# Performance work log

Measured on AMD Instinct MI355X. Metric: run time of the kernel, lower is better.

## Reference

```python
import jax, jax.numpy as jnp
import numpy as np
from jax import lax

B, CM, CQ, CO, H, W, KS = 8, 64, 64, 64, 128, 128, 3
K = KS * KS  # 9 kernel taps, offset_group=1


def setup_inputs() -> dict:
    key = jax.random.key(0)
    k1, k2, k3, k4 = jax.random.split(key, 4)
    mem = jax.random.normal(k1, (B, CM, H, W), jnp.float32)
    que = jax.random.normal(k2, (B, CQ, H, W), jnp.float32)
    # conv_offset: Conv2d(CM+CQ -> 3*K, 3x3, pad=1, bias=True); small init so offsets are a few px
    w_off = jax.random.normal(k3, (3 * K, CM + CQ, KS, KS), jnp.float32) * 0.01
    b_off = jnp.zeros((3 * K,), jnp.float32)
    # deformable conv weight: [CO, CM, 3, 3], bias=False
    w_def = jax.random.normal(k4, (CO, CM, KS, KS), jnp.float32) * (1.0 / np.sqrt(CM * K))
    return {"mem": mem, "que": que, "w_off": w_off, "b_off": b_off, "w_def": w_def}


def _deform_conv2d(mem, offset, mask, w_def):
    """Deformable conv v2 (stride=1, pad=1, dil=1, groups=1, offset_group=1).
    mem: [B,C,H,W]; offset: [B,2K,H,W] (dy,dx pairs per tap); mask: [B,K,H,W]."""
    Bn, C, Hn, Wn = mem.shape
    Kn = w_def.shape[2] * w_def.shape[3]
    off = offset.reshape(Bn, Kn, 2, Hn, Wn)
    dy, dx = off[:, :, 0], off[:, :, 1]            # [B,K,H,W]
    kk = jnp.arange(Kn)
    ky = (kk // KS - 1).astype(jnp.float32)        # kernel tap offsets with pad=1, dil=1
    kx = (kk % KS - 1).astype(jnp.float32)
    gy = jnp.arange(Hn, dtype=jnp.float32)
    gx = jnp.arange(Wn, dtype=jnp.float32)
    py = gy[None, None, :, None] + ky[None, :, None, None] + dy   # sample y coords [B,K,H,W]
    px = gx[None, None, None, :] + kx[None, :, None, None] + dx   # sample x coords [B,K,H,W]
    y0 = jnp.floor(py)
    x0 = jnp.floor(px)
    fy = py - y0
    fx = px - x0
    b_idx = jnp.arange(Bn)[:, None, None, None]

    def corner(iy, ix, wgt):
        valid = (iy >= 0) & (iy < Hn) & (ix >= 0) & (ix < Wn)  # zero padding outside
        iyc = jnp.clip(iy.astype(jnp.int32), 0, Hn - 1)
        ixc = jnp.clip(ix.astype(jnp.int32), 0, Wn - 1)
        vals = mem[b_idx, :, iyc, ixc]             # gather -> [B,K,H,W,C]
        return vals * (wgt * valid)[..., None]

    sampled = (corner(y0, x0, (1 - fy) * (1 - fx))
               + corner(y0, x0 + 1, (1 - fy) * fx)
               + corner(y0 + 1, x0, fy * (1 - fx))
               + corner(y0 + 1, x0 + 1, fy * fx))
    sampled = sampled * mask[..., None]            # modulation (applied raw, as in source)
    w = w_def.reshape(w_def.shape[0], C, Kn)       # [O,C,K]; tap order kh*KS+kw matches kk
    return jnp.einsum('bkhwc,ock->bohw', sampled, w)


def reference(mem, que, w_off, b_off, w_def):
    x = jnp.concatenate([mem, que], axis=1)
    off = lax.conv_general_dilated(
        x, w_off, window_strides=(1, 1), padding=[(1, 1), (1, 1)],
        dimension_numbers=('NCHW', 'OIHW', 'NCHW')) + b_off[None, :, None, None]
    offset, mask = off[:, :2 * K], off[:, 2 * K:]
    return _deform_conv2d(mem, offset, mask, w_def)
```

## Files before the change

### kernel.cpp

```cpp
#include <hip/hip_runtime.h>
#include <hip/hip_fp16.h>

#define Bn   8
#define CM_  64
#define CIN  128
#define CO_  64
#define Hn   128
#define Wn   128
#define Kn   9
#define COFF 27
#define HW   (Hn * Wn)

typedef __attribute__((ext_vector_type(8))) _Float16 f16x8;
typedef __attribute__((ext_vector_type(4))) float f32x4;

__device__ __forceinline__ unsigned h22u(__half2 h) {
    unsigned u; __builtin_memcpy(&u, &h, 4); return u;
}
__device__ __forceinline__ __half2 u2h2(unsigned u) {
    __half2 h; __builtin_memcpy(&h, &u, 4); return h;
}
__device__ __forceinline__ unsigned short f2h(float x) {
    __half h = __float2half(x);
    unsigned short u; __builtin_memcpy(&u, &h, 2); return u;
}

__global__ __launch_bounds__(256) void transpose_kernel(
    const float* __restrict__ mem, const float* __restrict__ que,
    uint4* __restrict__ xT4)
{
    __shared__ unsigned tile[64 * 65];

    const int bb   = blockIdx.x & 7;
    const int pix0 = (blockIdx.x >> 3) * 64;
    const int tid  = threadIdx.x;
    const int pxL  = tid & 63;
    const int cg   = tid >> 6;

    const float* mb = mem + (size_t)bb * CM_ * HW + pix0 + pxL;
    const float* qb = que + (size_t)bb * CM_ * HW + pix0 + pxL;

    #pragma unroll
    for (int i = 0; i < 16; ++i) {
        const int c = cg * 32 + 2 * i;
        const float v0 = (c < CM_) ? mb[(size_t)c * HW]       : qb[(size_t)(c - CM_) * HW];
        const float v1 = (c + 1 < CM_) ? mb[(size_t)(c + 1) * HW] : qb[(size_t)(c + 1 - CM_) * HW];
        tile[pxL * 65 + cg * 16 + i] = h22u(__floats2half2_rn(v0, v1));
    }
    __syncthreads();

    uint4* dst = xT4 + (size_t)(bb * HW + pix0) * 16;
    #pragma unroll
    for (int p = 0; p < 4; ++p) {
        const int G  = p * 256 + tid;
        const int px = G >> 4;
        const int u  = G & 15;
        uint4 v;
        v.x = tile[px * 65 + u * 4 + 0];
        v.y = tile[px * 65 + u * 4 + 1];
        v.z = tile[px * 65 + u * 4 + 2];
        v.w = tile[px * 65 + u * 4 + 3];
        dst[G] = v;
    }
}

__global__ __launch_bounds__(256) void wprep_all_kernel(
    const float* __restrict__ w_def, const float* __restrict__ w_off,
    unsigned short* __restrict__ wpd, unsigned short* __restrict__ wpo)
{
    int idx = blockIdx.x * 256 + threadIdx.x;
    if (idx < CO_ * CM_ * Kn) {
        const int j  = idx & 7;
        const int L  = (idx >> 3) & 63;
        const int f  = (idx >> 9) & 1;
        const int gk = idx >> 10;
        const int k  = gk % 9;
        const int g  = gk / 9;
        const int o  = g * 16 + (L & 15);
        const int c  = f * 32 + (L >> 4) * 8 + j;
        wpd[idx] = f2h(w_def[(size_t)(o * CM_ + c) * Kn + k]);
        return;
    }
    idx -= CO_ * CM_ * Kn;
    if (idx < 2 * 9 * 4 * 64 * 8) {
        const int j   = idx & 7;
        const int L   = (idx >> 3) & 63;
        const int s   = (idx >> 9) & 3;
        const int r   = idx >> 11;
        const int tap = r % 9;
        const int ot  = r / 9;
        const int o   = ot * 16 + (L & 15);
        const int c   = s * 32 + (L >> 4) * 8 + j;
        wpo[idx] = (o < COFF) ? f2h(w_off[(size_t)(o * CIN + c) * Kn + tap])
                              : (unsigned short)0;
    }
}

__global__ __launch_bounds__(256) void fused_deform_kernel(
    const uint4* __restrict__ xT4, const uint4* __restrict__ wpo,
    const uint4* __restrict__ wpd, const float* __restrict__ b_off,
    float* __restrict__ out)
{
    __shared__ __align__(16) char lds[198 * 16 * 16];
    uint4* xw   = (uint4*)lds;
    float* offl = (float*)lds;
    uint4* smp4 = (uint4*)(lds + 8192);

    const int bb   = blockIdx.x & 7;
    const int pix0 = (blockIdx.x >> 3) * 64;
    const int h0   = pix0 >> 7;
    const int w0   = pix0 & 127;
    const int tid  = threadIdx.x;
    const int wv   = tid >> 6;
    const int lane = tid & 63;
    const int quad = lane >> 4;
    const int lrow = lane & 15;

    const uint4* xb = xT4 + (size_t)bb * HW * 16;

    #pragma unroll
    for (int g = 0; g < 13; ++g) {
        const int idx = g * 256 + tid;
        if (idx < 198 * 16) {
            const int slot = idx >> 4;
            const int j    = idx & 15;
            const int r    = slot / 66;
            const int c    = slot - r * 66;
            const int y    = h0 + r - 1;
            const int x    = w0 + c - 1;
            const bool ok  = (y >= 0) & (y < Hn) & (x >= 0) & (x < Wn);
            uint4 v = make_uint4(0, 0, 0, 0);
            if (ok) v = xb[(size_t)(y * Wn + x) * 16 + j];
            xw[slot * 16 + (j ^ (slot & 7))] = v;
        }
    }
    __syncthreads();

    {
        const int ot   = wv >> 1;
        const int sub0 = (wv & 1) * 2;

        f32x4 oacc[2];
        #pragma unroll
        for (int t = 0; t < 2; ++t)
            #pragma unroll
            for (int r = 0; r < 4; ++r) {
                const int o = ot * 16 + quad * 4 + r;
                oacc[t][r] = (o < COFF) ? b_off[o] : 0.0f;
            }

        #pragma unroll
        for (int tap = 0; tap < 9; ++tap) {
            const int rr = tap / 3;
            const int cc = tap % 3;

            const uint4* ap = wpo + (size_t)((ot * 9 + tap) * 4) * 64 + lane;
            f16x8 a[4];
            #pragma unroll
            for (int s = 0; s < 4; ++s)
                a[s] = __builtin_bit_cast(f16x8, ap[s * 64]);

            #pragma unroll
            for (int t = 0; t < 2; ++t) {
                const int pl   = (sub0 + t) * 16 + lrow;
                const int slot = rr * 66 + pl + cc;
                const int base = slot * 16;
                const int sw   = slot & 7;
                #pragma unroll
                for (int s = 0; s < 4; ++s) {
                    const f16x8 bfrag = __builtin_bit_cast(f16x8,
                        xw[base + ((s * 4 + quad) ^ sw)]);
                    oacc[t] = __builtin_amdgcn_mfma_f32_16x16x32_f16(
                        a[s], bfrag, oacc[t], 0, 0, 0);
                }
            }
        }
        __syncthreads();

        #pragma unroll
        for (int t = 0; t < 2; ++t) {
            const int pl = (sub0 + t) * 16 + lrow;
            #pragma unroll
            for (int r = 0; r < 4; ++r) {
                const int o = ot * 16 + quad * 4 + r;
                if (o < COFF) offl[o * 64 + pl] = oacc[t][r];
            }
        }
        __syncthreads();
    }

    const int chunk = lane & 7;
    const int psub  = lane >> 3;

    const int pM = pix0 + lane;
    const int hM = pM >> 7;
    const int wM = pM & 127;

    f32x4 acc[4];
    #pragma unroll
    for (int i = 0; i < 4; ++i) acc[i] = (f32x4){0.f, 0.f, 0.f, 0.f};

    __half2 W00h[2], W01h[2], W10h[2], W11h[2];
    uint4   G00[2], G01[2], G10[2], G11[2];

    auto prep = [&](int k) {
        const float dy = offl[(2 * k    ) * 64 + lane];
        const float dx = offl[(2 * k + 1) * 64 + lane];
        const float mk = offl[(18 + k   ) * 64 + lane];
        const float py = (float)(hM + k / 3 - 1) + dy;
        const float px = (float)(wM + k % 3 - 1) + dx;
        const float y0f = floorf(py), x0f = floorf(px);
        const float fy = py - y0f,  fx = px - x0f;
        const int y0 = (int)y0f, x0 = (int)x0f;
        const int y1 = y0 + 1,   x1 = x0 + 1;
        const bool vy0 = (y0 >= 0) & (y0 < Hn);
        const bool vy1 = (y1 >= 0) & (y1 < Hn);
        const bool vx0 = (x0 >= 0) & (x0 < Wn);
        const bool vx1 = (x1 >= 0) & (x1 < Wn);
        const float w00 = (1.f - fy) * (1.f - fx) * (float)(vy0 & vx0) * mk;
        const float w01 = (1.f - fy) * fx         * (float)(vy0 & vx1) * mk;
        const float w10 = fy * (1.f - fx)         * (float)(vy1 & vx0) * mk;
        const float w11 = fy * fx                 * (float)(vy1 & vx1) * mk;
        const int y0c = min(max(y0, 0), Hn - 1);
        const int y1c = min(max(y1, 0), Hn - 1);
        const int x0c = min(max(x0, 0), Wn - 1);
        const int x1c = min(max(x1, 0), Wn - 1);
        const int i00 = y0c * Wn + x0c, i01 = y0c * Wn + x1c;
        const int i10 = y1c * Wn + x0c, i11 = y1c * Wn + x1c;

        #pragma unroll
        for (int g = 0; g < 2; ++g) {
            const int pl = g * 32 + wv * 8 + psub;
            W00h[g] = __float2half2_rn(__shfl(w00, pl, 64));
            W01h[g] = __float2half2_rn(__shfl(w01, pl, 64));
            W10h[g] = __float2half2_rn(__shfl(w10, pl, 64));
            W11h[g] = __float2half2_rn(__shfl(w11, pl, 64));
            const int I00 = __shfl(i00, pl, 64);
            const int I01 = __shfl(i01, pl, 64);
            const int I10 = __shfl(i10, pl, 64);
            const int I11 = __shfl(i11, pl, 64);
            G00[g] = xb[(size_t)I00 * 16 + chunk];
            G01[g] = xb[(size_t)I01 * 16 + chunk];
            G10[g] = xb[(size_t)I10 * 16 + chunk];
            G11[g] = xb[(size_t)I11 * 16 + chunk];
        }
    };

    auto blendwrite = [&](int buf) {
        #pragma unroll
        for (int g = 0; g < 2; ++g) {
            const int pl = g * 32 + wv * 8 + psub;
            const unsigned u00[4] = {G00[g].x, G00[g].y, G00[g].z, G00[g].w};
            const unsigned u01[4] = {G01[g].x, G01[g].y, G01[g].z, G01[g].w};
            const unsigned u10[4] = {G10[g].x, G10[g].y, G10[g].z, G10[g].w};
            const unsigned u11[4] = {G11[g].x, G11[g].y, G11[g].z, G11[g].w};
            unsigned pk[4];
            #pragma unroll
            for (int d = 0; d < 4; ++d) {
                __half2 s = __hmul2(u2h2(u00[d]), W00h[g]);
                s = __hfma2(u2h2(u01[d]), W01h[g], s);
                s = __hfma2(u2h2(u10[d]), W10h[g], s);
                s = __hfma2(u2h2(u11[d]), W11h[g], s);
                pk[d] = h22u(s);
            }
            smp4[buf * 512 + pl * 8 + (chunk ^ (pl & 7))] =
                make_uint4(pk[0], pk[1], pk[2], pk[3]);
        }
    };

    prep(0);
    blendwrite(0);
    __syncthreads();

    #pragma unroll
    for (int k = 0; k < Kn; ++k) {
        const int cur = k & 1;

        if (k < Kn - 1) prep(k + 1);

        const uint4* wpk = wpd + (size_t)((wv * 9 + k) * 2) * 64 + lane;
        const f16x8 a0 = __builtin_bit_cast(f16x8, wpk[0]);
        const f16x8 a1 = __builtin_bit_cast(f16x8, wpk[64]);

        #pragma unroll
        for (int nt = 0; nt < 4; ++nt) {
            const int pm = nt * 16 + lrow;
            const f16x8 b0 = __builtin_bit_cast(f16x8,
                smp4[cur * 512 + pm * 8 + ( quad      ^ (pm & 7))]);
            const f16x8 b1 = __builtin_bit_cast(f16x8,
                smp4[cur * 512 + pm * 8 + ((quad + 4) ^ (pm & 7))]);
            acc[nt] = __builtin_amdgcn_mfma_f32_16x16x32_f16(a0, b0, acc[nt], 0, 0, 0);
            acc[nt] = __builtin_amdgcn_mfma_f32_16x16x32_f16(a1, b1, acc[nt], 0, 0, 0);
        }

        if (k < Kn - 1) blendwrite(cur ^ 1);
        __syncthreads();
    }

    const int obase = (wv << 4) + (quad << 2);
    #pragma unroll
    for (int nt = 0; nt < 4; ++nt) {
        const int pp = pix0 + nt * 16 + lrow;
        #pragma unroll
        for (int r = 0; r < 4; ++r)
            out[(size_t)(bb * CO_ + obase + r) * HW + pp] = acc[nt][r];
    }
}

extern "C" void kernel_launch(void* const* d_in, const int* in_sizes, int n_in,
                              void* d_out, int out_size, void* d_ws, size_t ws_size,
                              hipStream_t stream) {
    const float* mem   = (const float*)d_in[0];
    const float* que   = (const float*)d_in[1];
    const float* w_off = (const float*)d_in[2];
    const float* b_off = (const float*)d_in[3];
    const float* w_def = (const float*)d_in[4];
    float* out = (float*)d_out;

    char* ws = (char*)d_ws;
    unsigned short* wpd = (unsigned short*)ws;
    unsigned short* wpo = (unsigned short*)(ws + 73728);
    uint4*          xT4 = (uint4*)(ws + 147456);

    transpose_kernel<<<2048, 256, 0, stream>>>(mem, que, xT4);
    wprep_all_kernel<<<288, 256, 0, stream>>>(w_def, w_off, wpd, wpo);
    fused_deform_kernel<<<2048, 256, 0, stream>>>(
        xT4, (const uint4*)wpo, (const uint4*)wpd, b_off, out);
}
```

Before: 172.9 us.

## Read offset-conv input tiles directly from global memory instead of LDS staging

Drops the cooperative LDS staging of the 3x66 input halo tile and its barrier. The offset-conv MFMA B fragments are now loaded straight from global memory, with the row skipped and the column masked at the borders. This cuts LDS footprint, so more blocks can be resident, and removes one sync. The cost is that each B fragment is fetched from global/L2 repeatedly, about three times across taps and across waves, rather than once into LDS.

```diff
diff --git a/kernel.cpp b/kernel.cpp
--- a/kernel.cpp
+++ b/kernel.cpp
@@ -101,8 +101,7 @@
     const uint4* __restrict__ wpd, const float* __restrict__ b_off,
     float* __restrict__ out)
 {
-    __shared__ __align__(16) char lds[198 * 16 * 16];
-    uint4* xw   = (uint4*)lds;
+    __shared__ __align__(16) char lds[24576];
     float* offl = (float*)lds;
     uint4* smp4 = (uint4*)(lds + 8192);
 
@@ -118,24 +117,6 @@
 
     const uint4* xb = xT4 + (size_t)bb * HW * 16;
 
-    #pragma unroll
-    for (int g = 0; g < 13; ++g) {
-        const int idx = g * 256 + tid;
-        if (idx < 198 * 16) {
-            const int slot = idx >> 4;
-            const int j    = idx & 15;
-            const int r    = slot / 66;
-            const int c    = slot - r * 66;
-            const int y    = h0 + r - 1;
-            const int x    = w0 + c - 1;
-            const bool ok  = (y >= 0) & (y < Hn) & (x >= 0) & (x < Wn);
-            uint4 v = make_uint4(0, 0, 0, 0);
-            if (ok) v = xb[(size_t)(y * Wn + x) * 16 + j];
-            xw[slot * 16 + (j ^ (slot & 7))] = v;
-        }
-    }
-    __syncthreads();
-
     {
         const int ot   = wv >> 1;
         const int sub0 = (wv & 1) * 2;
@@ -153,29 +134,31 @@
         for (int tap = 0; tap < 9; ++tap) {
             const int rr = tap / 3;
             const int cc = tap % 3;
-
-            const uint4* ap = wpo + (size_t)((ot * 9 + tap) * 4) * 64 + lane;
-            f16x8 a[4];
-            #pragma unroll
-            for (int s = 0; s < 4; ++s)
-                a[s] = __builtin_bit_cast(f16x8, ap[s * 64]);
-
-            #pragma unroll
-            for (int t = 0; t < 2; ++t) {
-                const int pl   = (sub0 + t) * 16 + lrow;
-                const int slot = rr * 66 + pl + cc;
-                const int base = slot * 16;
-                const int sw   = slot & 7;
+            const int y  = h0 + rr - 1;
+            if (y >= 0 && y < Hn) {
+                const uint4* ap = wpo + (size_t)((ot * 9 + tap) * 4) * 64 + lane;
+                f16x8 a[4];
                 #pragma unroll
-                for (int s = 0; s < 4; ++s) {
-                    const f16x8 bfrag = __builtin_bit_cast(f16x8,
-                        xw[base + ((s * 4 + quad) ^ sw)]);
-                    oacc[t] = __builtin_amdgcn_mfma_f32_16x16x32_f16(
-                        a[s], bfrag, oacc[t], 0, 0, 0);
+                for (int s = 0; s < 4; ++s)
+                    a[s] = __builtin_bit_cast(f16x8, ap[s * 64]);
+
+                #pragma unroll
+                for (int t = 0; t < 2; ++t) {
+                    const int pl   = (sub0 + t) * 16 + lrow;
+                    const int xcol = w0 + pl + cc - 1;
+                    const bool ok  = (xcol >= 0) & (xcol < Wn);
+                    const int xc   = min(max(xcol, 0), Wn - 1);
+                    const uint4* bp = xb + (size_t)(y * Wn + xc) * 16;
+                    #pragma unroll
+                    for (int s = 0; s < 4; ++s) {
+                        uint4 v = bp[s * 4 + quad];
+                        if (!ok) v = make_uint4(0, 0, 0, 0);
+                        oacc[t] = __builtin_amdgcn_mfma_f32_16x16x32_f16(
+                            a[s], __builtin_bit_cast(f16x8, v), oacc[t], 0, 0, 0);
+                    }
                 }
             }
         }
-        __syncthreads();
 
         #pragma unroll
         for (int t = 0; t < 2; ++t) {
@@ -235,10 +218,10 @@
             W01h[g] = __float2half2_rn(__shfl(w01, pl, 64));
             W10h[g] = __float2half2_rn(__shfl(w10, pl, 64));
             W11h[g] = __float2half2_rn(__shfl(w11, pl, 64));
-            const int I00 = __shfl(i00, pl, 64);
-            const int I01 = __shfl(i01, pl, 64);
-            const int I10 = __shfl(i10, pl, 64);
-            const int I11 = __shfl(i11, pl, 64);
+        const int I00 = __shfl(i00, pl, 64);
+        const int I01 = __shfl(i01, pl, 64);
+        const int I10 = __shfl(i10, pl, 64);
+        const int I11 = __shfl(i11, pl, 64);
             G00[g] = xb[(size_t)I00 * 16 + chunk];
             G01[g] = xb[(size_t)I01 * 16 + chunk];
             G10[g] = xb[(size_t)I10 * 16 + chunk];
```

After: 214.8 us. 24.2% more time.

## Deepen gather pipeline to two taps ahead and drop lane shuffles

Applied to the files above, without the earlier changes.

The bilinear gather loads are now issued two kernel taps ahead into a double-buffered register set, and the weight fragments are prefetched one tap ahead. This gives the global gathers more time to land before they are blended. Each lane now computes the coordinates and weights for its own pixels directly, replacing the cross-lane shuffles with redundant per-lane arithmetic. The final-iteration barrier is also removed. The extra in-flight registers (two sets of gather buffers) raise register pressure and could reduce occupancy.

```diff
diff --git a/kernel.cpp b/kernel.cpp
--- a/kernel.cpp
+++ b/kernel.cpp
@@ -192,109 +192,120 @@
     const int chunk = lane & 7;
     const int psub  = lane >> 3;
 
-    const int pM = pix0 + lane;
-    const int hM = pM >> 7;
-    const int wM = pM & 127;
+    int plg[2], hG[2], wG[2];
+    #pragma unroll
+    for (int g = 0; g < 2; ++g) {
+        plg[g] = g * 32 + wv * 8 + psub;
+        const int pG = pix0 + plg[g];
+        hG[g] = pG >> 7;
+        wG[g] = pG & 127;
+    }
 
     f32x4 acc[4];
     #pragma unroll
     for (int i = 0; i < 4; ++i) acc[i] = (f32x4){0.f, 0.f, 0.f, 0.f};
 
-    __half2 W00h[2], W01h[2], W10h[2], W11h[2];
-    uint4   G00[2], G01[2], G10[2], G11[2];
-
-    auto prep = [&](int k) {
-        const float dy = offl[(2 * k    ) * 64 + lane];
-        const float dx = offl[(2 * k + 1) * 64 + lane];
-        const float mk = offl[(18 + k   ) * 64 + lane];
-        const float py = (float)(hM + k / 3 - 1) + dy;
-        const float px = (float)(wM + k % 3 - 1) + dx;
-        const float y0f = floorf(py), x0f = floorf(px);
-        const float fy = py - y0f,  fx = px - x0f;
-        const int y0 = (int)y0f, x0 = (int)x0f;
-        const int y1 = y0 + 1,   x1 = x0 + 1;
-        const bool vy0 = (y0 >= 0) & (y0 < Hn);
-        const bool vy1 = (y1 >= 0) & (y1 < Hn);
-        const bool vx0 = (x0 >= 0) & (x0 < Wn);
-        const bool vx1 = (x1 >= 0) & (x1 < Wn);
-        const float w00 = (1.f - fy) * (1.f - fx) * (float)(vy0 & vx0) * mk;
-        const float w01 = (1.f - fy) * fx         * (float)(vy0 & vx1) * mk;
-        const float w10 = fy * (1.f - fx)         * (float)(vy1 & vx0) * mk;
-        const float w11 = fy * fx                 * (float)(vy1 & vx1) * mk;
-        const int y0c = min(max(y0, 0), Hn - 1);
-        const int y1c = min(max(y1, 0), Hn - 1);
-        const int x0c = min(max(x0, 0), Wn - 1);
-        const int x1c = min(max(x1, 0), Wn - 1);
-        const int i00 = y0c * Wn + x0c, i01 = y0c * Wn + x1c;
-        const int i10 = y1c * Wn + x0c, i11 = y1c * Wn + x1c;
-
+    uint4   GB[2][8];
+    __half2 WB[2][2][4];
+    f16x8   AF[2][2];
+
+    auto prep_issue = [&](int k) {
+        const int par = k & 1;
         #pragma unroll
         for (int g = 0; g < 2; ++g) {
-            const int pl = g * 32 + wv * 8 + psub;
-            W00h[g] = __float2half2_rn(__shfl(w00, pl, 64));
-            W01h[g] = __float2half2_rn(__shfl(w01, pl, 64));
-            W10h[g] = __float2half2_rn(__shfl(w10, pl, 64));
-            W11h[g] = __float2half2_rn(__shfl(w11, pl, 64));
-            const int I00 = __shfl(i00, pl, 64);
-            const int I01 = __shfl(i01, pl, 64);
-            const int I10 = __shfl(i10, pl, 64);
-            const int I11 = __shfl(i11, pl, 64);
-            G00[g] = xb[(size_t)I00 * 16 + chunk];
-            G01[g] = xb[(size_t)I01 * 16 + chunk];
-            G10[g] = xb[(size_t)I10 * 16 + chunk];
-            G11[g] = xb[(size_t)I11 * 16 + chunk];
+            const int pl = plg[g];
+            const float dy = offl[(2 * k    ) * 64 + pl];
+            const float dx = offl[(2 * k + 1) * 64 + pl];
+            const float mk = offl[(18 + k   ) * 64 + pl];
+            const float py  = (float)(hG[g] + k / 3 - 1) + dy;
+            const float pxf = (float)(wG[g] + k % 3 - 1) + dx;
+            const float y0f = floorf(py), x0f = floorf(pxf);
+            const float fy = py - y0f,  fx = pxf - x0f;
+            const int y0 = (int)y0f, x0 = (int)x0f;
+            const int y1 = y0 + 1,   x1 = x0 + 1;
+            const bool vy0 = (y0 >= 0) & (y0 < Hn);
+            const bool vy1 = (y1 >= 0) & (y1 < Hn);
+            const bool vx0 = (x0 >= 0) & (x0 < Wn);
+            const bool vx1 = (x1 >= 0) & (x1 < Wn);
+            const float w00 = (1.f - fy) * (1.f - fx) * (float)(vy0 & vx0) * mk;
+            const float w01 = (1.f - fy) * fx         * (float)(vy0 & vx1) * mk;
+            const float w10 = fy * (1.f - fx)         * (float)(vy1 & vx0) * mk;
+            const float w11 = fy * fx                 * (float)(vy1 & vx1) * mk;
+            WB[par][g][0] = __float2half2_rn(w00);
+            WB[par][g][1] = __float2half2_rn(w01);
+            WB[par][g][2] = __float2half2_rn(w10);
+            WB[par][g][3] = __float2half2_rn(w11);
+            const int y0c = min(max(y0, 0), Hn - 1);
+            const int y1c = min(max(y1, 0), Hn - 1);
+            const int x0c = min(max(x0, 0), Wn - 1);
+            const int x1c = min(max(x1, 0), Wn - 1);
+            const int i00 = y0c * Wn + x0c, i01 = y0c * Wn + x1c;
+            const int i10 = y1c * Wn + x0c, i11 = y1c * Wn + x1c;
+            GB[par][0 + g] = xb[(size_t)i00 * 16 + chunk];
+            GB[par][2 + g] = xb[(size_t)i01 * 16 + chunk];
+            GB[par][4 + g] = xb[(size_t)i10 * 16 + chunk];
+            GB[par][6 + g] = xb[(size_t)i11 * 16 + chunk];
         }
     };
 
-    auto blendwrite = [&](int buf) {
+    auto blend_store = [&](int k) {
+        const int par = k & 1;
         #pragma unroll
         for (int g = 0; g < 2; ++g) {
-            const int pl = g * 32 + wv * 8 + psub;
-            const unsigned u00[4] = {G00[g].x, G00[g].y, G00[g].z, G00[g].w};
-            const unsigned u01[4] = {G01[g].x, G01[g].y, G01[g].z, G01[g].w};
-            const unsigned u10[4] = {G10[g].x, G10[g].y, G10[g].z, G10[g].w};
-            const unsigned u11[4] = {G11[g].x, G11[g].y, G11[g].z, G11[g].w};
+            const int pl = plg[g];
+            const uint4 g00 = GB[par][0 + g], g01 = GB[par][2 + g];
+            const uint4 g10 = GB[par][4 + g], g11 = GB[par][6 + g];
+            const unsigned u00[4] = {g00.x, g00.y, g00.z, g00.w};
+            const unsigned u01[4] = {g01.x, g01.y, g01.z, g01.w};
+            const unsigned u10[4] = {g10.x, g10.y, g10.z, g10.w};
+            const unsigned u11[4] = {g11.x, g11.y, g11.z, g11.w};
             unsigned pk[4];
             #pragma unroll
             for (int d = 0; d < 4; ++d) {
-                __half2 s = __hmul2(u2h2(u00[d]), W00h[g]);
-                s = __hfma2(u2h2(u01[d]), W01h[g], s);
-                s = __hfma2(u2h2(u10[d]), W10h[g], s);
-                s = __hfma2(u2h2(u11[d]), W11h[g], s);
+                __half2 s = __hmul2(u2h2(u00[d]), WB[par][g][0]);
+                s = __hfma2(u2h2(u01[d]), WB[par][g][1], s);
+                s = __hfma2(u2h2(u10[d]), WB[par][g][2], s);
+                s = __hfma2(u2h2(u11[d]), WB[par][g][3], s);
                 pk[d] = h22u(s);
             }
-            smp4[buf * 512 + pl * 8 + (chunk ^ (pl & 7))] =
+            smp4[par * 512 + pl * 8 + (chunk ^ (pl & 7))] =
                 make_uint4(pk[0], pk[1], pk[2], pk[3]);
         }
     };
 
-    prep(0);
-    blendwrite(0);
+    auto load_af = [&](int k) {
+        const uint4* wpk = wpd + (size_t)((wv * 9 + k) * 2) * 64 + lane;
+        AF[k & 1][0] = __builtin_bit_cast(f16x8, wpk[0]);
+        AF[k & 1][1] = __builtin_bit_cast(f16x8, wpk[64]);
+    };
+
+    prep_issue(0);
+    prep_issue(1);
+    load_af(0);
+    blend_store(0);
     __syncthreads();
 
     #pragma unroll
-    for (int k = 0; k < Kn; ++k) {
-        const int cur = k & 1;
-
-        if (k < Kn - 1) prep(k + 1);
-
-        const uint4* wpk = wpd + (size_t)((wv * 9 + k) * 2) * 64 + lane;
-        const f16x8 a0 = __builtin_bit_cast(f16x8, wpk[0]);
-        const f16x8 a1 = __builtin_bit_cast(f16x8, wpk[64]);
-
+    for (int t = 0; t < Kn; ++t) {
+        if (t + 1 < Kn) load_af(t + 1);
+        if (t + 2 < Kn) prep_issue(t + 2);
+
+        const int buf = t & 1;
         #pragma unroll
         for (int nt = 0; nt < 4; ++nt) {
             const int pm = nt * 16 + lrow;
             const f16x8 b0 = __builtin_bit_cast(f16x8,
-                smp4[cur * 512 + pm * 8 + ( quad      ^ (pm & 7))]);
+                smp4[buf * 512 + pm * 8 + ( quad      ^ (pm & 7))]);
             const f16x8 b1 = __builtin_bit_cast(f16x8,
-                smp4[cur * 512 + pm * 8 + ((quad + 4) ^ (pm & 7))]);
-            acc[nt] = __builtin_amdgcn_mfma_f32_16x16x32_f16(a0, b0, acc[nt], 0, 0, 0);
-            acc[nt] = __builtin_amdgcn_mfma_f32_16x16x32_f16(a1, b1, acc[nt], 0, 0, 0);
-        }
-
-        if (k < Kn - 1) blendwrite(cur ^ 1);
-        __syncthreads();
+                smp4[buf * 512 + pm * 8 + ((quad + 4) ^ (pm & 7))]);
+            acc[nt] = __builtin_amdgcn_mfma_f32_16x16x32_f16(AF[buf][0], b0, acc[nt], 0, 0, 0);
+            acc[nt] = __builtin_amdgcn_mfma_f32_16x16x32_f16(AF[buf][1], b1, acc[nt], 0, 0, 0);
+        }
+
+        if (t + 1 < Kn) {
+            blend_store(t + 1);
+            __syncthreads();
+        }
     }
 
     const int obase = (wv << 4) + (quad << 2);
```

Result: faster. 166.0 us (-4.0%).
